# Kernel tuning notes

Hardware: AMD Instinct MI355X
Metric: run time of the kernel (lower is better)

The kernel has to match this reference:

```python
import jax, jax.numpy as jnp
import numpy as np

S = 50.0
M = 0.5
EPS = 1e-7
NORM_EPS = 1e-12

B, D = 1024, 512
C, K = 50000, 3


def _l2_normalize(x, axis=-1):
    n = jnp.linalg.norm(x, axis=axis, keepdims=True)
    return x / jnp.maximum(n, NORM_EPS)


def setup_inputs() -> dict:
    key = jax.random.key(0)
    k1, k2, k3 = jax.random.split(key, 3)
    embeddings = jax.random.normal(k1, (B, D), dtype=jnp.float32)
    labels = jax.random.randint(k2, (B,), 0, C, dtype=jnp.int64)
    # xavier_uniform over flattened (C*K, D) view
    limit = float(np.sqrt(6.0 / (C * K + D)))
    weight = jax.random.uniform(k3, (C, K, D), dtype=jnp.float32, minval=-limit, maxval=limit)
    return {"embeddings": embeddings, "labels": labels, "weight": weight}


def reference(embeddings, labels, weight):
    ne = _l2_normalize(embeddings, axis=-1)            # [B, D]
    nw = _l2_normalize(weight, axis=-1)                # [C, K, D] (row-wise over D)
    # cosine similarity expressed as a GEMM, then max over subcenters
    cosine = jnp.einsum('bd,ckd->bck', ne, nw)          # [B, C, K]
    cosine_max = jnp.max(cosine, axis=2)                # [B, C]
    theta = jnp.arccos(jnp.clip(cosine_max, -1.0 + EPS, 1.0 - EPS))
    target_logits = jnp.cos(theta + M)                  # [B, C]
    one_hot = jax.nn.one_hot(labels, C, dtype=cosine_max.dtype)
    return S * (one_hot * target_logits + (1.0 - one_hot) * cosine_max)
```

## Files before the change

### kernel.cpp

```cpp
#include <hip/hip_runtime.h>
#include <stdint.h>

#define B_N   1024
#define D_N   512
#define C_N   50000
#define K_N   3
#define CP    50016
#define NROWS (CP * 4)

#define S_SCALE 50.0f
#define COS_M   0.8775825619f
#define SIN_M   0.4794255386f
#define EPS_C   1e-7f

typedef __bf16 bf16_t;
typedef bf16_t bf16x8 __attribute__((ext_vector_type(8)));
typedef float  f32x4  __attribute__((ext_vector_type(4)));

__device__ __forceinline__ float wave_reduce_sum(float v) {
#pragma unroll
    for (int m = 1; m < 64; m <<= 1) v += __shfl_xor(v, m, 64);
    return v;
}

__device__ __forceinline__ void async_copy16(const void* g, void* l) {
    __builtin_amdgcn_global_load_lds(
        (const __attribute__((address_space(1))) void*)g,
        (__attribute__((address_space(3))) void*)l,
        16, 0, 0);
}

__global__ void k_norm_emb(const float* __restrict__ x, bf16_t* __restrict__ y) {
    const int row  = blockIdx.x * 4 + (threadIdx.x >> 6);
    const int lane = threadIdx.x & 63;
    const float4* p = (const float4*)(x + (size_t)row * D_N + lane * 8);
    float4 a = p[0], b = p[1];
    float s = a.x*a.x + a.y*a.y + a.z*a.z + a.w*a.w
            + b.x*b.x + b.y*b.y + b.z*b.z + b.w*b.w;
    s = wave_reduce_sum(s);
    float sc = 1.0f / fmaxf(sqrtf(s), 1e-12f);
    bf16x8 o;
    o[0] = (bf16_t)(a.x * sc); o[1] = (bf16_t)(a.y * sc);
    o[2] = (bf16_t)(a.z * sc); o[3] = (bf16_t)(a.w * sc);
    o[4] = (bf16_t)(b.x * sc); o[5] = (bf16_t)(b.y * sc);
    o[6] = (bf16_t)(b.z * sc); o[7] = (bf16_t)(b.w * sc);
    *(bf16x8*)(y + (size_t)row * D_N + lane * 8) = o;
}

__global__ void k_norm_w(const float* __restrict__ x, bf16_t* __restrict__ y) {
    const int row  = blockIdx.x * 4 + (threadIdx.x >> 6);
    const int lane = threadIdx.x & 63;
    const float4* p = (const float4*)(x + (size_t)row * D_N + lane * 8);
    float4 a = p[0], b = p[1];
    float s = a.x*a.x + a.y*a.y + a.z*a.z + a.w*a.w
            + b.x*b.x + b.y*b.y + b.z*b.z + b.w*b.w;
    s = wave_reduce_sum(s);
    float sc = 1.0f / fmaxf(sqrtf(s), 1e-12f);
    const size_t orow = (size_t)row + (size_t)(row / 3);
    bf16x8 o;
    o[0] = (bf16_t)(a.x * sc); o[1] = (bf16_t)(a.y * sc);
    o[2] = (bf16_t)(a.z * sc); o[3] = (bf16_t)(a.w * sc);
    o[4] = (bf16_t)(b.x * sc); o[5] = (bf16_t)(b.y * sc);
    o[6] = (bf16_t)(b.z * sc); o[7] = (bf16_t)(b.w * sc);
    *(bf16x8*)(y + orow * D_N + lane * 8) = o;
}

__global__ __launch_bounds__(256) void k_gemm(const bf16_t* __restrict__ Wn,
                                              const bf16_t* __restrict__ En,
                                              const int*    __restrict__ labels,
                                              float*        __restrict__ out) {
    __shared__ bf16_t Ws[128][32];
    __shared__ bf16_t Es[128][32];
    __shared__ float  So[128][33];

    const int tid  = threadIdx.x;
    const int wave = tid >> 6, lane = tid & 63;
    const int wr = wave >> 1, wc = wave & 1;
    const int col  = lane & 15, quad = lane >> 4;

    const int    b0 = blockIdx.x * 128;
    const size_t n0 = (size_t)blockIdx.y * 128;
    const int    c0 = blockIdx.y * 32;

    f32x4 acc[4][4] = {};

    const int srow   = lane >> 2;
    const int schunk = (lane & 3) * 8;

    for (int kk = 0; kk < D_N; kk += 32) {
        __syncthreads();
#pragma unroll
        for (int i = 0; i < 2; ++i) {
            const int rb = i * 64 + wave * 16;
            const bf16_t* ga = Wn + (n0 + rb + srow) * D_N + kk + schunk;
            async_copy16(ga, &Ws[rb][0]);
            const bf16_t* gb = En + (size_t)(b0 + rb + srow) * D_N + kk + schunk;
            async_copy16(gb, &Es[rb][0]);
        }
        __syncthreads();

        bf16x8 af[4], bfr[4];
#pragma unroll
        for (int t = 0; t < 4; ++t) {
            af[t]  = *(const bf16x8*)&Ws[wr * 64 + t * 16 + col][quad * 8];
            bfr[t] = *(const bf16x8*)&Es[wc * 64 + t * 16 + col][quad * 8];
        }
#pragma unroll
        for (int ti = 0; ti < 4; ++ti)
#pragma unroll
            for (int tj = 0; tj < 4; ++tj)
                acc[ti][tj] = __builtin_amdgcn_mfma_f32_16x16x32_bf16(
                    af[ti], bfr[tj], acc[ti][tj], 0, 0, 0);
    }

    int lab[4];
#pragma unroll
    for (int tj = 0; tj < 4; ++tj) lab[tj] = labels[b0 + wc * 64 + tj * 16 + col];

#pragma unroll
    for (int ti = 0; ti < 4; ++ti) {
        const int c_local = wr * 16 + ti * 4 + quad;
        const int c       = c0 + c_local;
#pragma unroll
        for (int tj = 0; tj < 4; ++tj) {
            float v = fmaxf(fmaxf(acc[ti][tj][0], acc[ti][tj][1]), acc[ti][tj][2]);
            if (c == lab[tj]) {
                float x = fminf(fmaxf(v, -1.0f + EPS_C), 1.0f - EPS_C);
                v = x * COS_M - sqrtf(fmaxf(1.0f - x * x, 0.0f)) * SIN_M;
            }
            So[wc * 64 + tj * 16 + col][c_local] = S_SCALE * v;
        }
    }
    __syncthreads();

    const int row  = tid >> 1;
    const int half = tid & 1;
    const size_t gbase = (size_t)(b0 + row) * C_N;
#pragma unroll
    for (int q = 0; q < 4; ++q) {
        const int ci = half * 16 + q * 4;
        const int c  = c0 + ci;
        if (c < C_N) {
            float4 o = make_float4(So[row][ci], So[row][ci + 1],
                                   So[row][ci + 2], So[row][ci + 3]);
            *(float4*)(out + gbase + c) = o;
        }
    }
}

__global__ void k_fb_norms(const float* __restrict__ emb, const float* __restrict__ w,
                           float* __restrict__ einv, float* __restrict__ winv) {
    const int row  = blockIdx.x * 4 + (threadIdx.x >> 6);
    const int lane = threadIdx.x & 63;
    if (row >= B_N + C_N * K_N) return;
    const float* src = (row < B_N) ? (emb + (size_t)row * D_N)
                                   : (w + (size_t)(row - B_N) * D_N);
    const float4* p = (const float4*)(src + lane * 8);
    float4 a = p[0], b = p[1];
    float s = a.x*a.x + a.y*a.y + a.z*a.z + a.w*a.w
            + b.x*b.x + b.y*b.y + b.z*b.z + b.w*b.w;
    s = wave_reduce_sum(s);
    if (lane == 0) {
        float sc = 1.0f / fmaxf(sqrtf(s), 1e-12f);
        if (row < B_N) einv[row] = sc; else winv[row - B_N] = sc;
    }
}

__global__ void k_fb_gemm(const float* __restrict__ emb, const float* __restrict__ w,
                          const int* __restrict__ labels, const float* __restrict__ einv,
                          const float* __restrict__ winv, float* __restrict__ out) {
    const int b = blockIdx.x;
    const int c = blockIdx.y * 256 + threadIdx.x;
    if (c >= C_N) return;
    const float4* e4 = (const float4*)(emb + (size_t)b * D_N);
    const float es = einv[b];
    float best = -1e30f;
    for (int k = 0; k < K_N; ++k) {
        const float4* w4 = (const float4*)(w + ((size_t)c * K_N + k) * D_N);
        float dot = 0.0f;
#pragma unroll 4
        for (int d = 0; d < D_N / 4; ++d) {
            float4 a = e4[d], bb = w4[d];
            dot += a.x*bb.x + a.y*bb.y + a.z*bb.z + a.w*bb.w;
        }
        dot *= es * winv[c * K_N + k];
        best = fmaxf(best, dot);
    }
    if (c == labels[b]) {
        float x = fminf(fmaxf(best, -1.0f + EPS_C), 1.0f - EPS_C);
        best = x * COS_M - sqrtf(fmaxf(1.0f - x * x, 0.0f)) * SIN_M;
    }
    out[(size_t)b * C_N + c] = S_SCALE * best;
}

extern "C" void kernel_launch(void* const* d_in, const int* in_sizes, int n_in,
                              void* d_out, int out_size, void* d_ws, size_t ws_size,
                              hipStream_t stream) {
    const float* emb    = (const float*)d_in[0];
    const int*   labels = (const int*)d_in[1];
    const float* weight = (const float*)d_in[2];
    float*       out    = (float*)d_out;

    const size_t offW = (size_t)1 << 20;
    const size_t need = offW + (size_t)NROWS * D_N * 2;
    if (ws_size >= need) {
        bf16_t* En = (bf16_t*)d_ws;
        bf16_t* Wn = (bf16_t*)((char*)d_ws + offW);
        k_norm_emb<<<B_N / 4, 256, 0, stream>>>(emb, En);
        k_norm_w<<<(C_N * K_N) / 4, 256, 0, stream>>>(weight, Wn);
        k_gemm<<<dim3(B_N / 128, NROWS / 128), 256, 0, stream>>>(Wn, En, labels, out);
    } else {
        float* einv = (float*)d_ws;
        float* winv = einv + B_N;
        k_fb_norms<<<(B_N + C_N * K_N) / 4, 256, 0, stream>>>(emb, weight, einv, winv);
        k_fb_gemm<<<dim3(B_N, (C_N + 255) / 256), 256, 0, stream>>>(emb, weight, labels,
                                                                    einv, winv, out);
    }
}
```

Before: 774.5 us.

## Replace GEMM with 256x256-tile, 8-wave double-buffered pipelined kernel

```diff
diff --git a/kernel.cpp b/kernel.cpp
--- a/kernel.cpp
+++ b/kernel.cpp
@@ -5,8 +5,8 @@
 #define D_N   512
 #define C_N   50000
 #define K_N   3
-#define CP    50016
-#define NROWS (CP * 4)
+#define CPAD  50048
+#define NROWS (CPAD * 4)
 
 #define S_SCALE 50.0f
 #define COS_M   0.8775825619f
@@ -48,102 +48,175 @@
 }
 
 __global__ void k_norm_w(const float* __restrict__ x, bf16_t* __restrict__ y) {
-    const int row  = blockIdx.x * 4 + (threadIdx.x >> 6);
+    const int w    = threadIdx.x >> 6;
     const int lane = threadIdx.x & 63;
-    const float4* p = (const float4*)(x + (size_t)row * D_N + lane * 8);
-    float4 a = p[0], b = p[1];
-    float s = a.x*a.x + a.y*a.y + a.z*a.z + a.w*a.w
-            + b.x*b.x + b.y*b.y + b.z*b.z + b.w*b.w;
-    s = wave_reduce_sum(s);
-    float sc = 1.0f / fmaxf(sqrtf(s), 1e-12f);
-    const size_t orow = (size_t)row + (size_t)(row / 3);
-    bf16x8 o;
-    o[0] = (bf16_t)(a.x * sc); o[1] = (bf16_t)(a.y * sc);
-    o[2] = (bf16_t)(a.z * sc); o[3] = (bf16_t)(a.w * sc);
-    o[4] = (bf16_t)(b.x * sc); o[5] = (bf16_t)(b.y * sc);
-    o[6] = (bf16_t)(b.z * sc); o[7] = (bf16_t)(b.w * sc);
-    *(bf16x8*)(y + orow * D_N + lane * 8) = o;
-}
-
-__global__ __launch_bounds__(256) void k_gemm(const bf16_t* __restrict__ Wn,
-                                              const bf16_t* __restrict__ En,
-                                              const int*    __restrict__ labels,
-                                              float*        __restrict__ out) {
-    __shared__ bf16_t Ws[128][32];
-    __shared__ bf16_t Es[128][32];
-    __shared__ float  So[128][33];
+    const int base = blockIdx.x * 16 + w * 4;
+#pragma unroll
+    for (int i = 0; i < 4; ++i) {
+        const int row = base + i;
+        const float4* p = (const float4*)(x + (size_t)row * D_N + lane * 8);
+        float4 a = p[0], b = p[1];
+        float s = a.x*a.x + a.y*a.y + a.z*a.z + a.w*a.w
+                + b.x*b.x + b.y*b.y + b.z*b.z + b.w*b.w;
+        s = wave_reduce_sum(s);
+        float sc = 1.0f / fmaxf(sqrtf(s), 1e-12f);
+        const size_t orow = (size_t)row + (size_t)(row / 3);
+        bf16x8 o;
+        o[0] = (bf16_t)(a.x * sc); o[1] = (bf16_t)(a.y * sc);
+        o[2] = (bf16_t)(a.z * sc); o[3] = (bf16_t)(a.w * sc);
+        o[4] = (bf16_t)(b.x * sc); o[5] = (bf16_t)(b.y * sc);
+        o[6] = (bf16_t)(b.z * sc); o[7] = (bf16_t)(b.w * sc);
+        *(bf16x8*)(y + orow * D_N + lane * 8) = o;
+    }
+}
+
+__global__ __launch_bounds__(512, 2) void k_gemm8(const bf16_t* __restrict__ Wn,
+                                                  const bf16_t* __restrict__ En,
+                                                  const int*    __restrict__ labels,
+                                                  float*        __restrict__ out) {
+    __shared__ __align__(16) char smem[131072];
 
     const int tid  = threadIdx.x;
-    const int wave = tid >> 6, lane = tid & 63;
-    const int wr = wave >> 1, wc = wave & 1;
-    const int col  = lane & 15, quad = lane >> 4;
-
-    const int    b0 = blockIdx.x * 128;
-    const size_t n0 = (size_t)blockIdx.y * 128;
-    const int    c0 = blockIdx.y * 32;
-
-    f32x4 acc[4][4] = {};
-
-    const int srow   = lane >> 2;
-    const int schunk = (lane & 3) * 8;
-
-    for (int kk = 0; kk < D_N; kk += 32) {
-        __syncthreads();
-#pragma unroll
-        for (int i = 0; i < 2; ++i) {
-            const int rb = i * 64 + wave * 16;
-            const bf16_t* ga = Wn + (n0 + rb + srow) * D_N + kk + schunk;
-            async_copy16(ga, &Ws[rb][0]);
-            const bf16_t* gb = En + (size_t)(b0 + rb + srow) * D_N + kk + schunk;
-            async_copy16(gb, &Es[rb][0]);
-        }
-        __syncthreads();
-
-        bf16x8 af[4], bfr[4];
-#pragma unroll
-        for (int t = 0; t < 4; ++t) {
-            af[t]  = *(const bf16x8*)&Ws[wr * 64 + t * 16 + col][quad * 8];
-            bfr[t] = *(const bf16x8*)&Es[wc * 64 + t * 16 + col][quad * 8];
-        }
-#pragma unroll
-        for (int ti = 0; ti < 4; ++ti)
-#pragma unroll
-            for (int tj = 0; tj < 4; ++tj)
-                acc[ti][tj] = __builtin_amdgcn_mfma_f32_16x16x32_bf16(
-                    af[ti], bfr[tj], acc[ti][tj], 0, 0, 0);
-    }
-
+    const int w    = tid >> 6;
+    const int lane = tid & 63;
+    const int wm   = w >> 2;
+    const int wn   = w & 3;
+    const int cl   = lane & 15;
+    const int quad = lane >> 4;
+
+    const int lid   = blockIdx.x;
+    const int nid   = (lid & 7) * 391 + (lid >> 3);
+    const int btile = nid & 3;
+    const int wtile = nid >> 2;
+    const int b0    = btile * 256;
+    const size_t r0 = (size_t)wtile * 256;
+
+    const int   srcswz = (((lane & 7) ^ (lane >> 3)) << 4);
+    const int   srow   = w * 8 + (lane >> 3);
+    const char* Wb = (const char*)Wn;
+    const char* Eb = (const char*)En;
+
+    auto stageA = [&](int tile, int h) {
+        char* l = smem + (tile & 1) * 65536 + h * 16384 + w * 1024;
+        const char* g = Wb + ((r0 + (size_t)(h * 128 + srow)) << 10) + tile * 128 + srcswz;
+        async_copy16(g, l);
+        async_copy16(g + (64 << 10), l + 8192);
+    };
+    auto stageB = [&](int tile, int h) {
+        char* l = smem + (tile & 1) * 65536 + 32768 + h * 16384 + w * 1024;
+        const char* g = Eb + ((size_t)(b0 + h * 128 + srow) << 10) + tile * 128 + srcswz;
+        async_copy16(g, l);
+        async_copy16(g + (64 << 10), l + 8192);
+    };
+
+    const int off0 = cl * 128 + ((      quad * 16) ^ ((lane & 7) << 4));
+    const int off1 = cl * 128 + ((64 +  quad * 16) ^ ((lane & 7) << 4));
+
+    f32x4  acc[8][4] = {};
+    bf16x8 a[4][2], b[4][2];
+
+    stageB(0, 0); stageB(0, 1); stageA(0, 0); stageA(0, 1);
+    asm volatile("s_waitcnt vmcnt(4)" ::: "memory");
+    stageB(1, 0); stageB(1, 1); stageA(1, 0);
+    asm volatile("s_waitcnt vmcnt(6)" ::: "memory");
+    __builtin_amdgcn_s_barrier();
+
+#define MFMA_QUAD(MB, NB)                                                        \
+    _Pragma("unroll")                                                            \
+    for (int mf = 0; mf < 4; ++mf) {                                             \
+        _Pragma("unroll")                                                        \
+        for (int nf = 0; nf < 2; ++nf) {                                         \
+            acc[(MB)*4+mf][(NB)*2+nf] = __builtin_amdgcn_mfma_f32_16x16x32_bf16( \
+                a[mf][0], b[(NB)*2+nf][0], acc[(MB)*4+mf][(NB)*2+nf], 0, 0, 0);  \
+            acc[(MB)*4+mf][(NB)*2+nf] = __builtin_amdgcn_mfma_f32_16x16x32_bf16( \
+                a[mf][1], b[(NB)*2+nf][1], acc[(MB)*4+mf][(NB)*2+nf], 0, 0, 0);  \
+        }                                                                        \
+    }
+
+#pragma unroll 2
+    for (int t = 0; t < 8; ++t) {
+        const char* Ab = smem + (t & 1) * 65536 + wm * 16384;
+        const char* Bb = smem + (t & 1) * 65536 + 32768 + (wn >> 1) * 16384 + (wn & 1) * 8192;
+
+#pragma unroll
+        for (int mf = 0; mf < 4; ++mf) {
+            a[mf][0] = *(const bf16x8*)(Ab + mf * 2048 + off0);
+            a[mf][1] = *(const bf16x8*)(Ab + mf * 2048 + off1);
+        }
+#pragma unroll
+        for (int nf = 0; nf < 4; ++nf) {
+            b[nf][0] = *(const bf16x8*)(Bb + nf * 2048 + off0);
+            b[nf][1] = *(const bf16x8*)(Bb + nf * 2048 + off1);
+        }
+        if (t < 7) stageA(t + 1, 1);
+        __builtin_amdgcn_s_barrier();
+        __builtin_amdgcn_s_setprio(1);
+        MFMA_QUAD(0, 0)
+        __builtin_amdgcn_s_setprio(0);
+        __builtin_amdgcn_s_barrier();
+
+        if (t < 6) stageB(t + 2, 0);
+        __builtin_amdgcn_s_barrier();
+        __builtin_amdgcn_s_setprio(1);
+        MFMA_QUAD(0, 1)
+        __builtin_amdgcn_s_setprio(0);
+        __builtin_amdgcn_s_barrier();
+
+#pragma unroll
+        for (int mf = 0; mf < 4; ++mf) {
+            a[mf][0] = *(const bf16x8*)(Ab + 8192 + mf * 2048 + off0);
+            a[mf][1] = *(const bf16x8*)(Ab + 8192 + mf * 2048 + off1);
+        }
+        if (t < 6) stageB(t + 2, 1);
+        __builtin_amdgcn_s_barrier();
+        __builtin_amdgcn_s_setprio(1);
+        MFMA_QUAD(1, 1)
+        __builtin_amdgcn_s_setprio(0);
+        __builtin_amdgcn_s_barrier();
+
+        if (t < 6) stageA(t + 2, 0);
+        __builtin_amdgcn_s_barrier();
+        __builtin_amdgcn_s_setprio(1);
+        MFMA_QUAD(1, 0)
+        __builtin_amdgcn_s_setprio(0);
+        if (t < 6)       { asm volatile("s_waitcnt vmcnt(6)" ::: "memory"); }
+        else if (t == 6) { asm volatile("s_waitcnt vmcnt(0)" ::: "memory"); }
+        __builtin_amdgcn_s_barrier();
+    }
+#undef MFMA_QUAD
+
+    float* So = (float*)smem;
     int lab[4];
 #pragma unroll
-    for (int tj = 0; tj < 4; ++tj) lab[tj] = labels[b0 + wc * 64 + tj * 16 + col];
-
-#pragma unroll
-    for (int ti = 0; ti < 4; ++ti) {
-        const int c_local = wr * 16 + ti * 4 + quad;
-        const int c       = c0 + c_local;
-#pragma unroll
-        for (int tj = 0; tj < 4; ++tj) {
-            float v = fmaxf(fmaxf(acc[ti][tj][0], acc[ti][tj][1]), acc[ti][tj][2]);
-            if (c == lab[tj]) {
+    for (int n = 0; n < 4; ++n) lab[n] = labels[b0 + wn * 64 + n * 16 + cl];
+
+    const int cb = wtile * 64;
+#pragma unroll
+    for (int m = 0; m < 8; ++m) {
+        const int cls_l = wm * 32 + (m >> 2) * 16 + (m & 3) * 4 + quad;
+        const int c = cb + cls_l;
+#pragma unroll
+        for (int n = 0; n < 4; ++n) {
+            float v = fmaxf(fmaxf(acc[m][n][0], acc[m][n][1]), acc[m][n][2]);
+            if (c == lab[n]) {
                 float x = fminf(fmaxf(v, -1.0f + EPS_C), 1.0f - EPS_C);
                 v = x * COS_M - sqrtf(fmaxf(1.0f - x * x, 0.0f)) * SIN_M;
             }
-            So[wc * 64 + tj * 16 + col][c_local] = S_SCALE * v;
+            So[(wn * 64 + n * 16 + cl) * 65 + cls_l] = S_SCALE * v;
         }
     }
     __syncthreads();
 
     const int row  = tid >> 1;
     const int half = tid & 1;
-    const size_t gbase = (size_t)(b0 + row) * C_N;
-#pragma unroll
-    for (int q = 0; q < 4; ++q) {
-        const int ci = half * 16 + q * 4;
-        const int c  = c0 + ci;
+    float*       gp = out + (size_t)(b0 + row) * C_N + cb + half * 32;
+    const float* sp = So + row * 65 + half * 32;
+#pragma unroll
+    for (int q = 0; q < 8; ++q) {
+        const int c = cb + half * 32 + q * 4;
         if (c < C_N) {
-            float4 o = make_float4(So[row][ci], So[row][ci + 1],
-                                   So[row][ci + 2], So[row][ci + 3]);
-            *(float4*)(out + gbase + c) = o;
+            float4 o = make_float4(sp[q*4+0], sp[q*4+1], sp[q*4+2], sp[q*4+3]);
+            *(float4*)(gp + q * 4) = o;
         }
     }
 }
@@ -207,8 +280,8 @@
         bf16_t* En = (bf16_t*)d_ws;
         bf16_t* Wn = (bf16_t*)((char*)d_ws + offW);
         k_norm_emb<<<B_N / 4, 256, 0, stream>>>(emb, En);
-        k_norm_w<<<(C_N * K_N) / 4, 256, 0, stream>>>(weight, Wn);
-        k_gemm<<<dim3(B_N / 128, NROWS / 128), 256, 0, stream>>>(Wn, En, labels, out);
+        k_norm_w<<<(C_N * K_N) / 16, 256, 0, stream>>>(weight, Wn);
+        k_gemm8<<<dim3(3128), 512, 0, stream>>>(Wn, En, labels, out);
     } else {
         float* einv = (float*)d_ws;
         float* winv = einv + B_N;
```

New measurement: 719.8 us. 1.08x faster.
